# Optimization experiments

Hardware: AMD Instinct MI355X
Metric: run time of the kernel (lower is better)

## Reference

```python
import jax, jax.numpy as jnp
import numpy as np

D, NH, T = 1024, 16, 2048
DH = D // NH
SCALE = 1.0 / np.sqrt(DH)


def setup_inputs() -> dict:
    key = jax.random.key(0)
    k1, k2, k3, k4 = jax.random.split(key, 4)
    x = jax.random.normal(k1, (4, T, D), dtype=jnp.float32)
    # torch nn.Linear weights: y = x @ W.T ; init scaled like default
    qkv_w = jax.random.normal(k2, (3 * D, D), dtype=jnp.float32) * (1.0 / np.sqrt(D))
    o_w = jax.random.normal(k3, (D, D), dtype=jnp.float32) * (1.0 / np.sqrt(D))
    o_b = jax.random.normal(k4, (D,), dtype=jnp.float32) * 0.01
    return {"x": x, "qkv_w": qkv_w, "o_w": o_w, "o_b": o_b}


def reference(x, qkv_w, o_w, o_b):
    b, t, c = x.shape
    qkv = jnp.einsum('btc,fc->btf', x, qkv_w)  # [b,t,3d]
    q, k, v = jnp.split(qkv, 3, axis=-1)
    # [b, nh, t, dh]
    q = q.reshape(b, t, NH, DH).transpose(0, 2, 1, 3)
    k = k.reshape(b, t, NH, DH).transpose(0, 2, 1, 3)
    v = v.reshape(b, t, NH, DH).transpose(0, 2, 1, 3)
    w = jnp.einsum('bhqd,bhkd->bhqk', q, k) * SCALE
    causal = jnp.tril(jnp.ones((t, t), dtype=bool))
    w = jnp.where(causal[None, None], w, -jnp.inf)
    w = jax.nn.softmax(w, axis=-1)
    out = jnp.einsum('bhqk,bhkd->bhqd', w, v)
    out = out.transpose(0, 2, 1, 3).reshape(b, t, c)
    return jnp.einsum('btc,oc->bto', out, o_w) + o_b
```

## Files before the change

kernel.cpp:

```cpp
#include <hip/hip_runtime.h>
#include <stdint.h>

#define TSEQ   2048
#define SCALE_K 0.18033688011112042f

typedef __attribute__((ext_vector_type(8))) short bf16x8;
typedef __attribute__((ext_vector_type(4))) short short4v;
typedef __attribute__((ext_vector_type(4))) float f32x4;

#define EXP2F(x) __builtin_amdgcn_exp2f(x)

__device__ __forceinline__ short f2bf(float f) {
  unsigned u = __float_as_uint(f);
  u = (u + 0x7fffu + ((u >> 16) & 1u)) >> 16;
  return (short)u;
}

__device__ __forceinline__ void async16(const void* gsrc, void* ldst) {
  __builtin_amdgcn_global_load_lds((__attribute__((address_space(1))) void*)(void*)gsrc,
                                   (__attribute__((address_space(3))) void*)ldst, 16, 0, 0);
}

__global__ void cast_f32_bf16(const float* __restrict__ src, short* __restrict__ dst, int n) {
  int i = (blockIdx.x * blockDim.x + threadIdx.x) * 4;
  if (i >= n) return;
  float4 v = *(const float4*)(src + i);
  short4v o;
  o[0] = f2bf(v.x); o[1] = f2bf(v.y); o[2] = f2bf(v.z); o[3] = f2bf(v.w);
  *(short4v*)(dst + i) = o;
}

template<int MODE>
__global__ __launch_bounds__(256, 2) void gemm_bt(
    const short* __restrict__ A, const short* __restrict__ B,
    void* __restrict__ C, short* __restrict__ Cvt, const float* __restrict__ bias,
    int M, int N, int K)
{
  __shared__ char ldsA[128 * 128];
  __shared__ char ldsB[128 * 128];

  const int tid  = threadIdx.x;
  const int lane = tid & 63;
  const int w    = tid >> 6;
  const int wrow = w >> 1, wcol = w & 1;
  const int l15  = lane & 15;
  const int klo  = (lane >> 4) << 4;

  int nwg = gridDim.x, orig = blockIdx.x;
  int qq = nwg >> 3, rr = nwg & 7;
  int xcd = orig & 7, lid = orig >> 3;
  int wgid = (xcd < rr ? xcd * (qq + 1) : rr * (qq + 1) + (xcd - rr) * qq) + lid;
  const int nbx = N >> 7;
  const int by = wgid / nbx, bx = wgid - by * nbx;
  const int m0 = by << 7, n0 = bx << 7;

  const char* Abase = (const char*)A + (size_t)m0 * K * 2;
  const char* Bbase = (const char*)B + (size_t)n0 * K * 2;
  const int rowstride = K * 2;

  const int srow  = tid >> 3;
  const int scolb = (tid & 7) << 4;

  f32x4 acc[4][4] = {};

  const int nk = K >> 6;
  for (int kk = 0; kk < nk; ++kk) {
    if (kk) __syncthreads();
    const int kbyte = kk << 7;
    #pragma unroll
    for (int p = 0; p < 4; ++p) {
      int row = p * 32 + srow;
      int sc  = scolb ^ ((row & 7) << 4);
      async16(Abase + (size_t)row * rowstride + kbyte + sc, ldsA + row * 128 + scolb);
      async16(Bbase + (size_t)row * rowstride + kbyte + sc, ldsB + row * 128 + scolb);
    }
    __syncthreads();

    bf16x8 af[2][4], bf[2][4];
    #pragma unroll
    for (int ks = 0; ks < 2; ++ks)
      #pragma unroll
      for (int mi = 0; mi < 4; ++mi) {
        int row = wrow * 64 + mi * 16 + l15;
        af[ks][mi] = *(const bf16x8*)(ldsA + row * 128 + ((ks * 64 + klo) ^ ((row & 7) << 4)));
      }
    #pragma unroll
    for (int ks = 0; ks < 2; ++ks)
      #pragma unroll
      for (int ni = 0; ni < 4; ++ni) {
        int row = wcol * 64 + ni * 16 + l15;
        bf[ks][ni] = *(const bf16x8*)(ldsB + row * 128 + ((ks * 64 + klo) ^ ((row & 7) << 4)));
      }
    #pragma unroll
    for (int mi = 0; mi < 4; ++mi)
      #pragma unroll
      for (int ni = 0; ni < 4; ++ni) {
        acc[mi][ni] = __builtin_amdgcn_mfma_f32_16x16x32_bf16(af[0][mi], bf[0][ni], acc[mi][ni], 0, 0, 0);
        acc[mi][ni] = __builtin_amdgcn_mfma_f32_16x16x32_bf16(af[1][mi], bf[1][ni], acc[mi][ni], 0, 0, 0);
      }
  }

  const int rbase = (lane >> 4) << 2;
  #pragma unroll
  for (int mi = 0; mi < 4; ++mi)
    #pragma unroll
    for (int ni = 0; ni < 4; ++ni) {
      const int col  = n0 + wcol * 64 + ni * 16 + l15;
      const int row0 = m0 + wrow * 64 + mi * 16 + rbase;
      if (MODE == 0) {
        #pragma unroll
        for (int j = 0; j < 4; ++j)
          ((float*)C)[(size_t)(row0 + j) * N + col] = acc[mi][ni][j] + bias[col];
      } else {
        if (n0 < 1024) {
          #pragma unroll
          for (int j = 0; j < 4; ++j)
            ((short*)C)[(size_t)(row0 + j) * 2048 + col] = f2bf(acc[mi][ni][j]);
        } else if (n0 < 2048) {
          #pragma unroll
          for (int j = 0; j < 4; ++j)
            ((short*)C)[(size_t)(row0 + j) * 2048 + col] = f2bf(acc[mi][ni][j] * SCALE_K);
        } else {
          short4v o;
          #pragma unroll
          for (int j = 0; j < 4; ++j) o[j] = f2bf(acc[mi][ni][j]);
          const int cv = col - 2048, hh = cv >> 6, dd = cv & 63;
          const int bb = row0 >> 11, t = row0 & 2047;
          *(short4v*)(Cvt + ((size_t)((bb * 16 + hh) * 64 + dd)) * 2048 + t) = o;
        }
      }
    }
}

__global__ __launch_bounds__(256, 3) void attn_wave(
    const short* __restrict__ qk, const short* __restrict__ vt, short* __restrict__ O)
{
  __shared__ short ldsP[4][32][72];

  const int tid  = threadIdx.x;
  const int lane = tid & 63;
  const int w    = tid >> 6;
  const int l15  = lane & 15;
  const int lg   = lane >> 4;
  short* ldsPw   = &ldsP[w][0][0];

  const int i  = blockIdx.x;
  const int qb = 63 - (i >> 4);
  const int bh = ((i & 15) << 2) + w;
  const int b  = bh >> 4, h = bh & 15;
  const int q0 = qb * 32;
  const int rowbase = b * TSEQ;

  const short* qbase = qk + (size_t)rowbase * 2048 + h * 64 + lg * 8;
  const short* kbase = qbase + 1024;
  const short* vbase = vt + ((size_t)bh * 64 + l15) * 2048 + lg * 8;

  bf16x8 qf[2][2];
  #pragma unroll
  for (int ks = 0; ks < 2; ++ks)
    #pragma unroll
    for (int qb2 = 0; qb2 < 2; ++qb2)
      qf[ks][qb2] = *(const bf16x8*)(qbase + (size_t)(q0 + qb2 * 16 + l15) * 2048 + ks * 32);

  f32x4 oacc[2][4] = {};
  float mrun[2] = {-1e30f, -1e30f}, lrun[2] = {0.f, 0.f};

  const int nst = (qb >> 1) + 1;
  for (int s = 0; s < nst; ++s) {
    const int kv0 = s * 64;

    bf16x8 kf[2][4];
    #pragma unroll
    for (int ks = 0; ks < 2; ++ks)
      #pragma unroll
      for (int kb = 0; kb < 4; ++kb)
        kf[ks][kb] = *(const bf16x8*)(kbase + (size_t)(kv0 + kb * 16 + l15) * 2048 + ks * 32);
    bf16x8 vf[2][4];
    #pragma unroll
    for (int c = 0; c < 2; ++c)
      #pragma unroll
      for (int ni = 0; ni < 4; ++ni)
        vf[c][ni] = *(const bf16x8*)(vbase + (size_t)(ni * 16) * 2048 + kv0 + c * 32);

    f32x4 sacc[4][2] = {};
    #pragma unroll
    for (int kb = 0; kb < 4; ++kb)
      #pragma unroll
      for (int qb2 = 0; qb2 < 2; ++qb2) {
        sacc[kb][qb2] = __builtin_amdgcn_mfma_f32_16x16x32_bf16(kf[0][kb], qf[0][qb2], sacc[kb][qb2], 0, 0, 0);
        sacc[kb][qb2] = __builtin_amdgcn_mfma_f32_16x16x32_bf16(kf[1][kb], qf[1][qb2], sacc[kb][qb2], 0, 0, 0);
      }

    if (s == nst - 1) {
      #pragma unroll
      for (int kb = 0; kb < 4; ++kb)
        #pragma unroll
        for (int qb2 = 0; qb2 < 2; ++qb2) {
          int qrow = q0 + qb2 * 16 + l15;
          #pragma unroll
          for (int j = 0; j < 4; ++j)
            if (kv0 + kb * 16 + lg * 4 + j > qrow) sacc[kb][qb2][j] = -1e30f;
        }
    }

    float alpha[2];
    #pragma unroll
    for (int qb2 = 0; qb2 < 2; ++qb2) {
      float t0 = fmaxf(fmaxf(sacc[0][qb2][0], sacc[0][qb2][1]), fmaxf(sacc[0][qb2][2], sacc[0][qb2][3]));
      float t1 = fmaxf(fmaxf(sacc[1][qb2][0], sacc[1][qb2][1]), fmaxf(sacc[1][qb2][2], sacc[1][qb2][3]));
      float t2 = fmaxf(fmaxf(sacc[2][qb2][0], sacc[2][qb2][1]), fmaxf(sacc[2][qb2][2], sacc[2][qb2][3]));
      float t3 = fmaxf(fmaxf(sacc[3][qb2][0], sacc[3][qb2][1]), fmaxf(sacc[3][qb2][2], sacc[3][qb2][3]));
      float v  = fmaxf(fmaxf(t0, t1), fmaxf(t2, t3));
      v = fmaxf(v, __shfl_xor(v, 16));
      v = fmaxf(v, __shfl_xor(v, 32));
      float mold = mrun[qb2];
      float mnew = fmaxf(mold, v);
      alpha[qb2] = EXP2F(mold - mnew);
      mrun[qb2]  = mnew;
      float rs = 0.f;
      #pragma unroll
      for (int kb = 0; kb < 4; ++kb) {
        float p0 = EXP2F(sacc[kb][qb2][0] - mnew);
        float p1 = EXP2F(sacc[kb][qb2][1] - mnew);
        float p2 = EXP2F(sacc[kb][qb2][2] - mnew);
        float p3 = EXP2F(sacc[kb][qb2][3] - mnew);
        rs += (p0 + p1) + (p2 + p3);
        short4v ps;
        ps[0] = f2bf(p0); ps[1] = f2bf(p1); ps[2] = f2bf(p2); ps[3] = f2bf(p3);
        *(short4v*)((char*)ldsPw + (qb2 * 16 + l15) * 144 + kb * 32 + lg * 8) = ps;
      }
      rs += __shfl_xor(rs, 16);
      rs += __shfl_xor(rs, 32);
      lrun[qb2] = lrun[qb2] * alpha[qb2] + rs;
    }

    #pragma unroll
    for (int mi = 0; mi < 2; ++mi)
      #pragma unroll
      for (int j = 0; j < 4; ++j) {
        float ar = __shfl(alpha[mi], lg * 4 + j);
        #pragma unroll
        for (int ni = 0; ni < 4; ++ni) oacc[mi][ni][j] *= ar;
      }

    asm volatile("" ::: "memory");

    bf16x8 pf[2][2];
    #pragma unroll
    for (int c = 0; c < 2; ++c)
      #pragma unroll
      for (int mi = 0; mi < 2; ++mi)
        pf[c][mi] = *(const bf16x8*)((const char*)ldsPw + (mi * 16 + l15) * 144 + c * 64 + lg * 16);

    asm volatile("" ::: "memory");

    #pragma unroll
    for (int mi = 0; mi < 2; ++mi)
      #pragma unroll
      for (int ni = 0; ni < 4; ++ni) {
        oacc[mi][ni] = __builtin_amdgcn_mfma_f32_16x16x32_bf16(pf[0][mi], vf[0][ni], oacc[mi][ni], 0, 0, 0);
        oacc[mi][ni] = __builtin_amdgcn_mfma_f32_16x16x32_bf16(pf[1][mi], vf[1][ni], oacc[mi][ni], 0, 0, 0);
      }
  }

  #pragma unroll
  for (int mi = 0; mi < 2; ++mi) {
    float linv = 1.0f / lrun[mi];
    #pragma unroll
    for (int j = 0; j < 4; ++j) {
      float lr = __shfl(linv, lg * 4 + j);
      int trow = rowbase + q0 + mi * 16 + lg * 4 + j;
      #pragma unroll
      for (int ni = 0; ni < 4; ++ni) {
        int col = h * 64 + ni * 16 + l15;
        O[(size_t)trow * 1024 + col] = f2bf(oacc[mi][ni][j] * lr);
      }
    }
  }
}

extern "C" void kernel_launch(void* const* d_in, const int* in_sizes, int n_in,
                              void* d_out, int out_size, void* d_ws, size_t ws_size,
                              hipStream_t stream) {
  const float* x     = (const float*)d_in[0];
  const float* qkv_w = (const float*)d_in[1];
  const float* o_w   = (const float*)d_in[2];
  const float* o_b   = (const float*)d_in[3];

  char* ws = (char*)d_ws;
  short* xb    = (short*)(ws);
  short* wqkvb = (short*)(ws + 16777216);
  short* wob   = (short*)(ws + 23068672);
  short* qkb   = (short*)(ws + 25165824);
  short* vtb   = (short*)(ws + 58720256);
  short* ob    = (short*)(ws + 75497472);

  cast_f32_bf16<<<8192, 256, 0, stream>>>(x,     xb,    8388608);
  cast_f32_bf16<<<3072, 256, 0, stream>>>(qkv_w, wqkvb, 3145728);
  cast_f32_bf16<<<1024, 256, 0, stream>>>(o_w,   wob,   1048576);

  gemm_bt<2><<<1536, 256, 0, stream>>>(xb, wqkvb, (void*)qkb, vtb, nullptr, 8192, 3072, 1024);

  attn_wave<<<1024, 256, 0, stream>>>(qkb, vtb, ob);

  gemm_bt<0><<<512, 256, 0, stream>>>(ob, wob, d_out, nullptr, o_b, 8192, 1024, 1024);
}
```

Measured before the change: 225.4 us.

## Use 16-row query tiles paired for causal balance and prefetch next K tile

Each wave now handles two 16-row query tiles (qp and 127-qp) instead of one 32-row tile, so causal work per wave is uniform and load is balanced across blocks. The block index mapping is changed to spread batch-heads across consecutive blocks. The next K tile is loaded right after the QK MFMAs so its fetch overlaps the softmax. Occupancy is raised to 4 blocks per SIMD via launch bounds, and the LDS P buffer is halved. In exchange, reuse of each K/V load drops because only 16 query rows share it, which roughly doubles K/V traffic per query.

```diff
diff --git a/kernel.cpp b/kernel.cpp
--- a/kernel.cpp
+++ b/kernel.cpp
@@ -132,10 +132,10 @@
     }
 }
 
-__global__ __launch_bounds__(256, 3) void attn_wave(
+__global__ __launch_bounds__(256, 4) void attn_wave(
     const short* __restrict__ qk, const short* __restrict__ vt, short* __restrict__ O)
 {
-  __shared__ short ldsP[4][32][72];
+  __shared__ short ldsP[4][16][72];
 
   const int tid  = threadIdx.x;
   const int lane = tid & 63;
@@ -145,138 +145,133 @@
   short* ldsPw   = &ldsP[w][0][0];
 
   const int i  = blockIdx.x;
-  const int qb = 63 - (i >> 4);
-  const int bh = ((i & 15) << 2) + w;
+  const int bh = (i & 7) * 8 + ((i >> 3) & 7);
+  const int qp = ((i >> 6) & 15) * 4 + w;
   const int b  = bh >> 4, h = bh & 15;
-  const int q0 = qb * 32;
   const int rowbase = b * TSEQ;
 
   const short* qbase = qk + (size_t)rowbase * 2048 + h * 64 + lg * 8;
   const short* kbase = qbase + 1024;
   const short* vbase = vt + ((size_t)bh * 64 + l15) * 2048 + lg * 8;
 
-  bf16x8 qf[2][2];
-  #pragma unroll
-  for (int ks = 0; ks < 2; ++ks)
-    #pragma unroll
-    for (int qb2 = 0; qb2 < 2; ++qb2)
-      qf[ks][qb2] = *(const bf16x8*)(qbase + (size_t)(q0 + qb2 * 16 + l15) * 2048 + ks * 32);
-
-  f32x4 oacc[2][4] = {};
-  float mrun[2] = {-1e30f, -1e30f}, lrun[2] = {0.f, 0.f};
-
-  const int nst = (qb >> 1) + 1;
-  for (int s = 0; s < nst; ++s) {
-    const int kv0 = s * 64;
+  auto run_tile = [&](int qt) {
+    const int q0 = qt * 16;
+
+    bf16x8 qf[2];
+    #pragma unroll
+    for (int ks = 0; ks < 2; ++ks)
+      qf[ks] = *(const bf16x8*)(qbase + (size_t)(q0 + l15) * 2048 + ks * 32);
+
+    f32x4 oacc[4] = {};
+    float mrun = -1e30f, lrun = 0.f;
+    const int nst = (qt >> 2) + 1;
 
     bf16x8 kf[2][4];
     #pragma unroll
     for (int ks = 0; ks < 2; ++ks)
       #pragma unroll
       for (int kb = 0; kb < 4; ++kb)
-        kf[ks][kb] = *(const bf16x8*)(kbase + (size_t)(kv0 + kb * 16 + l15) * 2048 + ks * 32);
-    bf16x8 vf[2][4];
-    #pragma unroll
-    for (int c = 0; c < 2; ++c)
-      #pragma unroll
-      for (int ni = 0; ni < 4; ++ni)
-        vf[c][ni] = *(const bf16x8*)(vbase + (size_t)(ni * 16) * 2048 + kv0 + c * 32);
-
-    f32x4 sacc[4][2] = {};
-    #pragma unroll
-    for (int kb = 0; kb < 4; ++kb)
-      #pragma unroll
-      for (int qb2 = 0; qb2 < 2; ++qb2) {
-        sacc[kb][qb2] = __builtin_amdgcn_mfma_f32_16x16x32_bf16(kf[0][kb], qf[0][qb2], sacc[kb][qb2], 0, 0, 0);
-        sacc[kb][qb2] = __builtin_amdgcn_mfma_f32_16x16x32_bf16(kf[1][kb], qf[1][qb2], sacc[kb][qb2], 0, 0, 0);
-      }
-
-    if (s == nst - 1) {
-      #pragma unroll
-      for (int kb = 0; kb < 4; ++kb)
-        #pragma unroll
-        for (int qb2 = 0; qb2 < 2; ++qb2) {
-          int qrow = q0 + qb2 * 16 + l15;
+        kf[ks][kb] = *(const bf16x8*)(kbase + (size_t)(kb * 16 + l15) * 2048 + ks * 32);
+
+    for (int s = 0; s < nst; ++s) {
+      const int kv0 = s * 64;
+
+      bf16x8 vf[2][4];
+      #pragma unroll
+      for (int c = 0; c < 2; ++c)
+        #pragma unroll
+        for (int ni = 0; ni < 4; ++ni)
+          vf[c][ni] = *(const bf16x8*)(vbase + (size_t)(ni * 16) * 2048 + kv0 + c * 32);
+
+      f32x4 sacc[4] = {};
+      #pragma unroll
+      for (int kb = 0; kb < 4; ++kb) {
+        sacc[kb] = __builtin_amdgcn_mfma_f32_16x16x32_bf16(kf[0][kb], qf[0], sacc[kb], 0, 0, 0);
+        sacc[kb] = __builtin_amdgcn_mfma_f32_16x16x32_bf16(kf[1][kb], qf[1], sacc[kb], 0, 0, 0);
+      }
+
+      if (s + 1 < nst) {
+        #pragma unroll
+        for (int ks = 0; ks < 2; ++ks)
+          #pragma unroll
+          for (int kb = 0; kb < 4; ++kb)
+            kf[ks][kb] = *(const bf16x8*)(kbase + (size_t)(kv0 + 64 + kb * 16 + l15) * 2048 + ks * 32);
+      }
+
+      if (s == nst - 1) {
+        const int qrow = q0 + l15;
+        #pragma unroll
+        for (int kb = 0; kb < 4; ++kb)
           #pragma unroll
           for (int j = 0; j < 4; ++j)
-            if (kv0 + kb * 16 + lg * 4 + j > qrow) sacc[kb][qb2][j] = -1e30f;
-        }
-    }
-
-    float alpha[2];
-    #pragma unroll
-    for (int qb2 = 0; qb2 < 2; ++qb2) {
-      float t0 = fmaxf(fmaxf(sacc[0][qb2][0], sacc[0][qb2][1]), fmaxf(sacc[0][qb2][2], sacc[0][qb2][3]));
-      float t1 = fmaxf(fmaxf(sacc[1][qb2][0], sacc[1][qb2][1]), fmaxf(sacc[1][qb2][2], sacc[1][qb2][3]));
-      float t2 = fmaxf(fmaxf(sacc[2][qb2][0], sacc[2][qb2][1]), fmaxf(sacc[2][qb2][2], sacc[2][qb2][3]));
-      float t3 = fmaxf(fmaxf(sacc[3][qb2][0], sacc[3][qb2][1]), fmaxf(sacc[3][qb2][2], sacc[3][qb2][3]));
+            if (kv0 + kb * 16 + lg * 4 + j > qrow) sacc[kb][j] = -1e30f;
+      }
+
+      float t0 = fmaxf(fmaxf(sacc[0][0], sacc[0][1]), fmaxf(sacc[0][2], sacc[0][3]));
+      float t1 = fmaxf(fmaxf(sacc[1][0], sacc[1][1]), fmaxf(sacc[1][2], sacc[1][3]));
+      float t2 = fmaxf(fmaxf(sacc[2][0], sacc[2][1]), fmaxf(sacc[2][2], sacc[2][3]));
+      float t3 = fmaxf(fmaxf(sacc[3][0], sacc[3][1]), fmaxf(sacc[3][2], sacc[3][3]));
       float v  = fmaxf(fmaxf(t0, t1), fmaxf(t2, t3));
       v = fmaxf(v, __shfl_xor(v, 16));
       v = fmaxf(v, __shfl_xor(v, 32));
-      float mold = mrun[qb2];
+      float mold = mrun;
       float mnew = fmaxf(mold, v);
-      alpha[qb2] = EXP2F(mold - mnew);
-      mrun[qb2]  = mnew;
+      float alpha = EXP2F(mold - mnew);
+      mrun = mnew;
       float rs = 0.f;
       #pragma unroll
       for (int kb = 0; kb < 4; ++kb) {
-        float p0 = EXP2F(sacc[kb][qb2][0] - mnew);
-        float p1 = EXP2F(sacc[kb][qb2][1] - mnew);
-        float p2 = EXP2F(sacc[kb][qb2][2] - mnew);
-        float p3 = EXP2F(sacc[kb][qb2][3] - mnew);
+        float p0 = EXP2F(sacc[kb][0] - mnew);
+        float p1 = EXP2F(sacc[kb][1] - mnew);
+        float p2 = EXP2F(sacc[kb][2] - mnew);
+        float p3 = EXP2F(sacc[kb][3] - mnew);
         rs += (p0 + p1) + (p2 + p3);
         short4v ps;
         ps[0] = f2bf(p0); ps[1] = f2bf(p1); ps[2] = f2bf(p2); ps[3] = f2bf(p3);
-        *(short4v*)((char*)ldsPw + (qb2 * 16 + l15) * 144 + kb * 32 + lg * 8) = ps;
+        *(short4v*)((char*)ldsPw + l15 * 144 + kb * 32 + lg * 8) = ps;
       }
       rs += __shfl_xor(rs, 16);
       rs += __shfl_xor(rs, 32);
-      lrun[qb2] = lrun[qb2] * alpha[qb2] + rs;
+      lrun = lrun * alpha + rs;
+
+      #pragma unroll
+      for (int j = 0; j < 4; ++j) {
+        float ar = __shfl(alpha, lg * 4 + j);
+        #pragma unroll
+        for (int ni = 0; ni < 4; ++ni) oacc[ni][j] *= ar;
+      }
+
+      asm volatile("" ::: "memory");
+
+      bf16x8 pf[2];
+      #pragma unroll
+      for (int c = 0; c < 2; ++c)
+        pf[c] = *(const bf16x8*)((const char*)ldsPw + l15 * 144 + c * 64 + lg * 16);
+
+      asm volatile("" ::: "memory");
+
+      #pragma unroll
+      for (int ni = 0; ni < 4; ++ni) {
+        oacc[ni] = __builtin_amdgcn_mfma_f32_16x16x32_bf16(pf[0], vf[0][ni], oacc[ni], 0, 0, 0);
+        oacc[ni] = __builtin_amdgcn_mfma_f32_16x16x32_bf16(pf[1], vf[1][ni], oacc[ni], 0, 0, 0);
+      }
     }
 
-    #pragma unroll
-    for (int mi = 0; mi < 2; ++mi)
-      #pragma unroll
-      for (int j = 0; j < 4; ++j) {
-        float ar = __shfl(alpha[mi], lg * 4 + j);
-        #pragma unroll
-        for (int ni = 0; ni < 4; ++ni) oacc[mi][ni][j] *= ar;
-      }
-
-    asm volatile("" ::: "memory");
-
-    bf16x8 pf[2][2];
-    #pragma unroll
-    for (int c = 0; c < 2; ++c)
-      #pragma unroll
-      for (int mi = 0; mi < 2; ++mi)
-        pf[c][mi] = *(const bf16x8*)((const char*)ldsPw + (mi * 16 + l15) * 144 + c * 64 + lg * 16);
-
-    asm volatile("" ::: "memory");
-
-    #pragma unroll
-    for (int mi = 0; mi < 2; ++mi)
-      #pragma unroll
-      for (int ni = 0; ni < 4; ++ni) {
-        oacc[mi][ni] = __builtin_amdgcn_mfma_f32_16x16x32_bf16(pf[0][mi], vf[0][ni], oacc[mi][ni], 0, 0, 0);
-        oacc[mi][ni] = __builtin_amdgcn_mfma_f32_16x16x32_bf16(pf[1][mi], vf[1][ni], oacc[mi][ni], 0, 0, 0);
-      }
-  }
-
-  #pragma unroll
-  for (int mi = 0; mi < 2; ++mi) {
-    float linv = 1.0f / lrun[mi];
+    float linv = 1.0f / lrun;
     #pragma unroll
     for (int j = 0; j < 4; ++j) {
       float lr = __shfl(linv, lg * 4 + j);
-      int trow = rowbase + q0 + mi * 16 + lg * 4 + j;
+      int trow = rowbase + q0 + lg * 4 + j;
       #pragma unroll
       for (int ni = 0; ni < 4; ++ni) {
         int col = h * 64 + ni * 16 + l15;
-        O[(size_t)trow * 1024 + col] = f2bf(oacc[mi][ni][j] * lr);
+        O[(size_t)trow * 1024 + col] = f2bf(oacc[ni][j] * lr);
       }
     }
-  }
+  };
+
+  run_tile(qp);
+  run_tile(127 - qp);
 }
 
 extern "C" void kernel_launch(void* const* d_in, const int* in_sizes, int n_in,
```

After: 346.8 us. 1.54x slower.

## Keep softmax probabilities in registers and compute transposed PV MFMA

Applied to the files above, without the earlier changes.

The attention kernel drops the LDS round-trip for the P matrix. It packs exp values into bf16 registers with v_cvt_pk_bf16_f32 and feeds them straight into a transposed O^T = V^T·P^T MFMA, which also removes the alpha shuffles. V fragments are now gathered as two 8-byte loads so their layout matches the register-resident P. The output store becomes vectorized along rows, and launch bounds rise to 4 blocks per CU. In exchange, V reads are narrower and the occupancy request may constrain registers.

```diff
diff --git a/kernel.cpp b/kernel.cpp
--- a/kernel.cpp
+++ b/kernel.cpp
@@ -14,6 +14,12 @@
   unsigned u = __float_as_uint(f);
   u = (u + 0x7fffu + ((u >> 16) & 1u)) >> 16;
   return (short)u;
+}
+
+__device__ __forceinline__ unsigned cvt_pk_bf16(float lo, float hi) {
+  unsigned r;
+  asm("v_cvt_pk_bf16_f32 %0, %1, %2" : "=v"(r) : "v"(lo), "v"(hi));
+  return r;
 }
 
 __device__ __forceinline__ void async16(const void* gsrc, void* ldst) {
@@ -132,17 +138,14 @@
     }
 }
 
-__global__ __launch_bounds__(256, 3) void attn_wave(
+__global__ __launch_bounds__(256, 4) void attn_wave(
     const short* __restrict__ qk, const short* __restrict__ vt, short* __restrict__ O)
 {
-  __shared__ short ldsP[4][32][72];
-
   const int tid  = threadIdx.x;
   const int lane = tid & 63;
   const int w    = tid >> 6;
   const int l15  = lane & 15;
   const int lg   = lane >> 4;
-  short* ldsPw   = &ldsP[w][0][0];
 
   const int i  = blockIdx.x;
   const int qb = 63 - (i >> 4);
@@ -153,7 +156,7 @@
 
   const short* qbase = qk + (size_t)rowbase * 2048 + h * 64 + lg * 8;
   const short* kbase = qbase + 1024;
-  const short* vbase = vt + ((size_t)bh * 64 + l15) * 2048 + lg * 8;
+  const short* vtb   = vt + (size_t)bh * 64 * 2048;
 
   bf16x8 qf[2][2];
   #pragma unroll
@@ -175,12 +178,20 @@
       #pragma unroll
       for (int kb = 0; kb < 4; ++kb)
         kf[ks][kb] = *(const bf16x8*)(kbase + (size_t)(kv0 + kb * 16 + l15) * 2048 + ks * 32);
+
     bf16x8 vf[2][4];
     #pragma unroll
-    for (int c = 0; c < 2; ++c)
-      #pragma unroll
-      for (int ni = 0; ni < 4; ++ni)
-        vf[c][ni] = *(const bf16x8*)(vbase + (size_t)(ni * 16) * 2048 + kv0 + c * 32);
+    for (int ks = 0; ks < 2; ++ks)
+      #pragma unroll
+      for (int ni = 0; ni < 4; ++ni) {
+        const short* vrow = vtb + (size_t)(ni * 16 + l15) * 2048 + kv0 + ks * 32 + lg * 4;
+        short4v a0 = *(const short4v*)(vrow);
+        short4v a1 = *(const short4v*)(vrow + 16);
+        bf16x8 vv;
+        vv[0] = a0[0]; vv[1] = a0[1]; vv[2] = a0[2]; vv[3] = a0[3];
+        vv[4] = a1[0]; vv[5] = a1[1]; vv[6] = a1[2]; vv[7] = a1[3];
+        vf[ks][ni] = vv;
+      }
 
     f32x4 sacc[4][2] = {};
     #pragma unroll
@@ -203,7 +214,6 @@
         }
     }
 
-    float alpha[2];
     #pragma unroll
     for (int qb2 = 0; qb2 < 2; ++qb2) {
       float t0 = fmaxf(fmaxf(sacc[0][qb2][0], sacc[0][qb2][1]), fmaxf(sacc[0][qb2][2], sacc[0][qb2][3]));
@@ -215,9 +225,11 @@
       v = fmaxf(v, __shfl_xor(v, 32));
       float mold = mrun[qb2];
       float mnew = fmaxf(mold, v);
-      alpha[qb2] = EXP2F(mold - mnew);
-      mrun[qb2]  = mnew;
+      float alpha = EXP2F(mold - mnew);
+      mrun[qb2] = mnew;
+
       float rs = 0.f;
+      bf16x8 pf[2];
       #pragma unroll
       for (int kb = 0; kb < 4; ++kb) {
         float p0 = EXP2F(sacc[kb][qb2][0] - mnew);
@@ -225,56 +237,39 @@
         float p2 = EXP2F(sacc[kb][qb2][2] - mnew);
         float p3 = EXP2F(sacc[kb][qb2][3] - mnew);
         rs += (p0 + p1) + (p2 + p3);
-        short4v ps;
-        ps[0] = f2bf(p0); ps[1] = f2bf(p1); ps[2] = f2bf(p2); ps[3] = f2bf(p3);
-        *(short4v*)((char*)ldsPw + (qb2 * 16 + l15) * 144 + kb * 32 + lg * 8) = ps;
+        unsigned w0 = cvt_pk_bf16(p0, p1);
+        unsigned w1 = cvt_pk_bf16(p2, p3);
+        pf[kb >> 1][(kb & 1) * 4 + 0] = (short)(w0 & 0xffff);
+        pf[kb >> 1][(kb & 1) * 4 + 1] = (short)(w0 >> 16);
+        pf[kb >> 1][(kb & 1) * 4 + 2] = (short)(w1 & 0xffff);
+        pf[kb >> 1][(kb & 1) * 4 + 3] = (short)(w1 >> 16);
       }
       rs += __shfl_xor(rs, 16);
       rs += __shfl_xor(rs, 32);
-      lrun[qb2] = lrun[qb2] * alpha[qb2] + rs;
-    }
-
-    #pragma unroll
-    for (int mi = 0; mi < 2; ++mi)
-      #pragma unroll
-      for (int j = 0; j < 4; ++j) {
-        float ar = __shfl(alpha[mi], lg * 4 + j);
-        #pragma unroll
-        for (int ni = 0; ni < 4; ++ni) oacc[mi][ni][j] *= ar;
-      }
-
-    asm volatile("" ::: "memory");
-
-    bf16x8 pf[2][2];
-    #pragma unroll
-    for (int c = 0; c < 2; ++c)
-      #pragma unroll
-      for (int mi = 0; mi < 2; ++mi)
-        pf[c][mi] = *(const bf16x8*)((const char*)ldsPw + (mi * 16 + l15) * 144 + c * 64 + lg * 16);
-
-    asm volatile("" ::: "memory");
-
-    #pragma unroll
-    for (int mi = 0; mi < 2; ++mi)
+      lrun[qb2] = lrun[qb2] * alpha + rs;
+
       #pragma unroll
       for (int ni = 0; ni < 4; ++ni) {
-        oacc[mi][ni] = __builtin_amdgcn_mfma_f32_16x16x32_bf16(pf[0][mi], vf[0][ni], oacc[mi][ni], 0, 0, 0);
-        oacc[mi][ni] = __builtin_amdgcn_mfma_f32_16x16x32_bf16(pf[1][mi], vf[1][ni], oacc[mi][ni], 0, 0, 0);
-      }
+        oacc[qb2][ni][0] *= alpha; oacc[qb2][ni][1] *= alpha;
+        oacc[qb2][ni][2] *= alpha; oacc[qb2][ni][3] *= alpha;
+        oacc[qb2][ni] = __builtin_amdgcn_mfma_f32_16x16x32_bf16(vf[0][ni], pf[0], oacc[qb2][ni], 0, 0, 0);
+        oacc[qb2][ni] = __builtin_amdgcn_mfma_f32_16x16x32_bf16(vf[1][ni], pf[1], oacc[qb2][ni], 0, 0, 0);
+      }
+    }
   }
 
   #pragma unroll
-  for (int mi = 0; mi < 2; ++mi) {
-    float linv = 1.0f / lrun[mi];
-    #pragma unroll
-    for (int j = 0; j < 4; ++j) {
-      float lr = __shfl(linv, lg * 4 + j);
-      int trow = rowbase + q0 + mi * 16 + lg * 4 + j;
-      #pragma unroll
-      for (int ni = 0; ni < 4; ++ni) {
-        int col = h * 64 + ni * 16 + l15;
-        O[(size_t)trow * 1024 + col] = f2bf(oacc[mi][ni][j] * lr);
-      }
+  for (int qb2 = 0; qb2 < 2; ++qb2) {
+    float linv = 1.0f / lrun[qb2];
+    const size_t rowoff = (size_t)(rowbase + q0 + qb2 * 16 + l15) * 1024 + h * 64 + lg * 4;
+    #pragma unroll
+    for (int ni = 0; ni < 4; ++ni) {
+      short4v o;
+      o[0] = f2bf(oacc[qb2][ni][0] * linv);
+      o[1] = f2bf(oacc[qb2][ni][1] * linv);
+      o[2] = f2bf(oacc[qb2][ni][2] * linv);
+      o[3] = f2bf(oacc[qb2][ni][3] * linv);
+      *(short4v*)(O + rowoff + ni * 16) = o;
     }
   }
 }
```

Result: slower. 331.6 us (+47.1%).
